# Kernel optimization log

Measured on AMD Instinct MI355X. Metric: run time of the kernel, lower is better.

Reference implementation:

```python
import jax, jax.numpy as jnp
import numpy as np

N_NODES = 50000
N_EDGES = 640000
IN_CH = 64
EDGE_DIM = 16
HID = 128
OUT = 128
L = 5
N_GRAPHS = 128
BN_EPS = 1e-5


def setup_inputs() -> dict:
    key = jax.random.key(0)
    ks = jax.random.split(key, 16)

    def w(k, shape, fan_in):
        return jax.random.normal(k, shape, jnp.float32) / np.sqrt(fan_in)

    inp = {}
    inp["x"] = jax.random.normal(ks[0], (N_NODES, IN_CH), jnp.float32)
    inp["edge_index"] = jax.random.randint(ks[1], (2, N_EDGES), 0, N_NODES)
    inp["edge_attr"] = jax.random.normal(ks[2], (N_EDGES, EDGE_DIM), jnp.float32)
    inp["batch"] = jnp.sort(jax.random.randint(ks[3], (N_NODES,), 0, N_GRAPHS))
    # node / edge encoders
    inp["node_w"] = w(ks[4], (IN_CH, HID), IN_CH)
    inp["node_b"] = jnp.zeros((HID,), jnp.float32)
    inp["edge_w"] = w(ks[5], (EDGE_DIM, HID), EDGE_DIM)
    inp["edge_b"] = jnp.zeros((HID,), jnp.float32)
    # per-layer GINEConv params (stacked over L layers)
    inp["eps"] = jnp.zeros((L,), jnp.float32)  # train_eps init 0
    inp["lin_w"] = w(ks[6], (L, HID, HID), HID)       # GINEConv internal edge lin
    inp["lin_b"] = jnp.zeros((L, HID), jnp.float32)
    inp["mlp1_w"] = w(ks[7], (L, HID, 2 * HID), HID)
    inp["mlp1_b"] = jnp.zeros((L, 2 * HID), jnp.float32)
    inp["mlp2_w"] = w(ks[8], (L, 2 * HID, HID), 2 * HID)
    inp["mlp2_b"] = jnp.zeros((L, HID), jnp.float32)
    inp["bn_g"] = jnp.ones((L, HID), jnp.float32)
    inp["bn_b"] = jnp.zeros((L, HID), jnp.float32)
    # output MLP: HID -> HID//2 -> OUT
    inp["out_w1"] = w(ks[9], (HID, HID // 2), HID)
    inp["out_b1"] = jnp.zeros((HID // 2,), jnp.float32)
    inp["out_w2"] = w(ks[10], (HID // 2, OUT), HID // 2)
    inp["out_b2"] = jnp.zeros((OUT,), jnp.float32)
    return inp


def reference(x, edge_index, edge_attr, batch, node_w, node_b, edge_w, edge_b,
              eps, lin_w, lin_b, mlp1_w, mlp1_b, mlp2_w, mlp2_b, bn_g, bn_b,
              out_w1, out_b1, out_w2, out_b2):
    n_nodes = x.shape[0]
    src, dst = edge_index[0], edge_index[1]
    # node / edge encoders (dropout is identity in eval)
    h = jax.nn.relu(x @ node_w + node_b)            # [N, H]
    e = edge_attr @ edge_w + edge_b                  # [E, H]
    n_layers = lin_w.shape[0]
    for l in range(n_layers):
        # GINEConv: message = relu(x_src + lin(edge_emb)); aggregate = scatter-sum to dst
        m = jax.nn.relu(h[src] + e @ lin_w[l] + lin_b[l])      # [E, H]
        agg = jax.ops.segment_sum(m, dst, num_segments=n_nodes)  # [N, H]
        z = (1.0 + eps[l]) * h + agg
        # GINE MLP: H -> 2H -> H
        z = jax.nn.relu(z @ mlp1_w[l] + mlp1_b[l]) @ mlp2_w[l] + mlp2_b[l]
        # BatchNorm over nodes (training-mode batch statistics)
        mu = z.mean(axis=0)
        var = z.var(axis=0)
        z = (z - mu) * jax.lax.rsqrt(var + BN_EPS) * bn_g[l] + bn_b[l]
        # residual then relu
        h = jax.nn.relu(z + h)
    # global mean pool per graph
    counts = jax.ops.segment_sum(jnp.ones((n_nodes,), h.dtype), batch, num_segments=N_GRAPHS)
    pooled = jax.ops.segment_sum(h, batch, num_segments=N_GRAPHS) / jnp.maximum(counts, 1.0)[:, None]
    # output MLP (dropout identity in eval)
    logits = jax.nn.relu(pooled @ out_w1 + out_b1) @ out_w2 + out_b2
    return (logits, pooled)
```

## Files before the change

### kernel.cpp

```cpp
#include <hip/hip_runtime.h>

#define N_NODES  50000
#define NPAD     50048
#define N_EDGES  640000
#define IN_CH    64
#define EDGE_DIM 16
#define HID      128
#define HID2     256
#define NLAYER   5
#define NGRAPH   128
#define MT64     (NPAD / 64)

typedef unsigned short ushort_t;
typedef __attribute__((ext_vector_type(8))) short short8;
typedef __attribute__((ext_vector_type(4))) short s16x4;
typedef __attribute__((ext_vector_type(4))) float f32x4;
typedef __attribute__((ext_vector_type(2))) float f32x2;

__device__ __forceinline__ float b2f(ushort_t u) {
    union { unsigned v; float f; } x; x.v = ((unsigned)u) << 16; return x.f;
}
__device__ __forceinline__ ushort_t f2b(float f) {
    union { float f; unsigned u; } x; x.f = f;
    unsigned u = x.u;
    unsigned r = (u + 0x7FFFu + ((u >> 16) & 1u)) >> 16;
    return (ushort_t)r;
}

__global__ void k_transpose_cvt(const float* __restrict__ src, ushort_t* __restrict__ dst,
                                int B, int K, int Nn) {
    long total = (long)B * K * Nn;
    for (long i = (long)blockIdx.x * blockDim.x + threadIdx.x; i < total;
         i += (long)gridDim.x * blockDim.x) {
        int b = (int)(i / ((long)K * Nn));
        int rem = (int)(i - (long)b * K * Nn);
        int k = rem / Nn;
        int n = rem - k * Nn;
        dst[(long)b * K * Nn + (long)n * K + k] = f2b(src[i]);
    }
}

__global__ __launch_bounds__(128) void k_combine(const float* __restrict__ ew,
                                                 const float* __restrict__ eb,
                                                 const float* __restrict__ lw,
                                                 const float* __restrict__ lb,
                                                 ushort_t* __restrict__ WcbT,
                                                 float* __restrict__ cc) {
    int l = blockIdx.x, j = threadIdx.x;
    float accW[EDGE_DIM];
#pragma unroll
    for (int k = 0; k < EDGE_DIM; ++k) accW[k] = 0.f;
    float accc = 0.f;
    for (int i = 0; i < HID; ++i) {
        float lwv = lw[((long)l * HID + i) * HID + j];
        accc = fmaf(eb[i], lwv, accc);
#pragma unroll
        for (int k = 0; k < EDGE_DIM; ++k)
            accW[k] = fmaf(ew[k * HID + i], lwv, accW[k]);
    }
    ushort_t* wp = WcbT + ((long)l * HID + j) * 32;
#pragma unroll
    for (int k = 0; k < EDGE_DIM; ++k) wp[k] = f2b(accW[k]);
#pragma unroll
    for (int k = EDGE_DIM; k < 32; ++k) wp[k] = 0;
    cc[l * HID + j] = accc + lb[l * HID + j];
}

__global__ __launch_bounds__(256) void k_hist(const int* __restrict__ ei, int* __restrict__ deg) {
    int e = blockIdx.x * 256 + threadIdx.x;
    if (e < N_EDGES) atomicAdd(&deg[ei[N_EDGES + e]], 1);
}

__global__ __launch_bounds__(1024) void k_scan1(const int* __restrict__ deg,
                                                int* __restrict__ offs, int* __restrict__ bsum) {
    __shared__ int s[1024];
    int i = blockIdx.x * 1024 + threadIdx.x;
    int v = (i < N_NODES) ? deg[i] : 0;
    s[threadIdx.x] = v;
    __syncthreads();
    for (int off = 1; off < 1024; off <<= 1) {
        int t = (threadIdx.x >= off) ? s[threadIdx.x - off] : 0;
        __syncthreads();
        s[threadIdx.x] += t;
        __syncthreads();
    }
    if (i < N_NODES) offs[i] = s[threadIdx.x] - v;
    if (threadIdx.x == 1023) bsum[blockIdx.x] = s[1023];
}

__global__ void k_scan2(int* __restrict__ bsum, int nb) {
    if (threadIdx.x == 0 && blockIdx.x == 0) {
        int acc = 0;
        for (int i = 0; i < nb; ++i) { int v = bsum[i]; bsum[i] = acc; acc += v; }
    }
}

__global__ __launch_bounds__(1024) void k_scan3(int* __restrict__ offs, const int* __restrict__ bsum) {
    int i = blockIdx.x * 1024 + threadIdx.x;
    if (i < N_NODES) offs[i] += bsum[blockIdx.x];
}

__global__ __launch_bounds__(256) void k_scatter(const int* __restrict__ ei,
                                                 const float* __restrict__ ea,
                                                 const int* __restrict__ offs,
                                                 int* __restrict__ cursor,
                                                 int* __restrict__ src_s,
                                                 ushort_t* __restrict__ ea_sb) {
    int e = blockIdx.x * 256 + threadIdx.x;
    if (e >= N_EDGES) return;
    int d = ei[N_EDGES + e];
    int pos = offs[d] + atomicAdd(&cursor[d], 1);
    src_s[pos] = ei[e];
    const f32x4* srcp = (const f32x4*)(ea + (long)e * EDGE_DIM);
    f32x4 v0 = srcp[0], v1 = srcp[1], v2 = srcp[2], v3 = srcp[3];
    short8 o0, o1;
#pragma unroll
    for (int j = 0; j < 4; ++j) {
        o0[j] = (short)f2b(v0[j]); o0[4 + j] = (short)f2b(v1[j]);
        o1[j] = (short)f2b(v2[j]); o1[4 + j] = (short)f2b(v3[j]);
    }
    short8* dst = (short8*)(ea_sb + (long)pos * EDGE_DIM);
    dst[0] = o0;
    dst[1] = o1;
}

__global__ __launch_bounds__(256) void k_node_enc(const float* __restrict__ x,
                                                  const ushort_t* __restrict__ w0T,
                                                  const float* __restrict__ nb,
                                                  float* __restrict__ h,
                                                  ushort_t* __restrict__ hb) {
    __shared__ __align__(16) short lB[HID * IN_CH];
    for (int c = threadIdx.x; c < HID * IN_CH / 8; c += 256) {
        int row = c >> 3, k0 = (c & 7) * 8;
        short8 v = *(const short8*)(w0T + row * IN_CH + k0);
        int g = (k0 >> 3) ^ (row & 7);
        *(short8*)&lB[row * IN_CH + g * 8] = v;
    }
    __syncthreads();
    int wv = threadIdx.x >> 6, l6 = threadIdx.x & 63;
    int lr = l6 & 15, lg = l6 >> 4;
    int grow = blockIdx.x * 64 + wv * 16 + lr;
    f32x4 acc[8];
#pragma unroll
    for (int nt = 0; nt < 8; ++nt) acc[nt] = (f32x4){0.f, 0.f, 0.f, 0.f};
#pragma unroll
    for (int kt = 0; kt < 2; ++kt) {
        int kk = kt * 32 + lg * 8;
        short8 a = {0, 0, 0, 0, 0, 0, 0, 0};
        if (grow < N_NODES) {
            const float* xr = x + (long)grow * IN_CH + kk;
            f32x4 v0 = *(const f32x4*)xr;
            f32x4 v1 = *(const f32x4*)(xr + 4);
#pragma unroll
            for (int j = 0; j < 4; ++j) { a[j] = (short)f2b(v0[j]); a[4 + j] = (short)f2b(v1[j]); }
        }
#pragma unroll
        for (int nt = 0; nt < 8; ++nt) {
            int brow = nt * 16 + lr;
            short8 b = *(const short8*)&lB[brow * IN_CH + (((kk >> 3) ^ (brow & 7)) << 3)];
            acc[nt] = __builtin_amdgcn_mfma_f32_16x16x32_bf16(a, b, acc[nt], 0, 0, 0);
        }
    }
    int orow0 = blockIdx.x * 64 + wv * 16 + lg * 4;
#pragma unroll
    for (int nt = 0; nt < 8; ++nt) {
        int col = nt * 16 + lr;
        float bias = nb[col];
#pragma unroll
        for (int r = 0; r < 4; ++r) {
            int row = orow0 + r;
            if (row < N_NODES) {
                float v = fmaxf(acc[nt][r] + bias, 0.f);
                h[(long)row * HID + col] = v;
                hb[(long)row * HID + col] = f2b(v);
            }
        }
    }
}

__global__ __launch_bounds__(256) void k_edgegemm(const ushort_t* __restrict__ ea_sb,
                                                  const ushort_t* __restrict__ WcbT,
                                                  const float* __restrict__ cc,
                                                  ushort_t* __restrict__ g, int l,
                                                  int ce0, int ce1) {
    int wv = threadIdx.x >> 6, l6 = threadIdx.x & 63;
    int lr = l6 & 15, lg = l6 >> 4;
    short8 af[8];
    f32x4 cv[8];
    const ushort_t* wp = WcbT + (long)l * HID * 32;
#pragma unroll
    for (int nt = 0; nt < 8; ++nt) {
        af[nt] = *(const short8*)(wp + (nt * 16 + lr) * 32 + lg * 8);
        cv[nt] = *(const f32x4*)(cc + l * HID + nt * 16 + lg * 4);
    }
    for (int it = 0; it < 4; ++it) {
        int e0 = ce0 + blockIdx.x * 256 + wv * 64 + it * 16;
        int e = e0 + lr;
        short8 b = {0, 0, 0, 0, 0, 0, 0, 0};
        if (e < ce1 && lg < 2) b = *(const short8*)(ea_sb + (long)e * EDGE_DIM + lg * 8);
        f32x4 acc[8];
#pragma unroll
        for (int nt = 0; nt < 8; ++nt) acc[nt] = (f32x4){0.f, 0.f, 0.f, 0.f};
#pragma unroll
        for (int nt = 0; nt < 8; ++nt)
            acc[nt] = __builtin_amdgcn_mfma_f32_16x16x32_bf16(af[nt], b, acc[nt], 0, 0, 0);
        if (e < ce1) {
            ushort_t* gp = g + (long)(e - ce0) * HID + lg * 4;
#pragma unroll
            for (int nt = 0; nt < 8; ++nt) {
                s16x4 o;
#pragma unroll
                for (int r = 0; r < 4; ++r) o[r] = (short)f2b(acc[nt][r] + cv[nt][r]);
                *(s16x4*)(gp + nt * 16) = o;
            }
        }
    }
}

__global__ __launch_bounds__(256) void k_edge2(const ushort_t* __restrict__ g,
                                               const int* __restrict__ src_s,
                                               const int* __restrict__ offs,
                                               const int* __restrict__ deg,
                                               const float* __restrict__ h,
                                               const ushort_t* __restrict__ hb,
                                               const float* __restrict__ epsv,
                                               float* __restrict__ zacc,
                                               ushort_t* __restrict__ z,
                                               int l, int ce0, int ce1, int mode) {
    int lane = threadIdx.x & 63;
    int node = blockIdx.x * 4 + (threadIdx.x >> 6);
    if (node >= N_NODES) return;
    bool first = mode & 1, last = (mode & 2) != 0;
    int ch0 = lane * 2;
    int s0 = offs[node];
    int dg = deg[node];
    int e_lo = max(s0, ce0);
    int e_hi = min(s0 + dg, ce1);
    if (e_lo >= e_hi && !first && !last) return;
    float a0 = 0.f, a1 = 0.f;
    int i = e_lo;
    for (; i + 4 <= e_hi; i += 4) {
        long eg = (long)(i - ce0);
        int sa = src_s[i], sb_ = src_s[i + 1], sc_ = src_s[i + 2], sd_ = src_s[i + 3];
        unsigned ga = *(const unsigned*)(g + eg * HID + ch0);
        unsigned gb = *(const unsigned*)(g + (eg + 1) * HID + ch0);
        unsigned gc = *(const unsigned*)(g + (eg + 2) * HID + ch0);
        unsigned gd = *(const unsigned*)(g + (eg + 3) * HID + ch0);
        unsigned ha = *(const unsigned*)(hb + (long)sa * HID + ch0);
        unsigned hbv = *(const unsigned*)(hb + (long)sb_ * HID + ch0);
        unsigned hc = *(const unsigned*)(hb + (long)sc_ * HID + ch0);
        unsigned hd = *(const unsigned*)(hb + (long)sd_ * HID + ch0);
        a0 += fmaxf(b2f((ushort_t)(ha & 0xffff)) + b2f((ushort_t)(ga & 0xffff)), 0.f);
        a1 += fmaxf(b2f((ushort_t)(ha >> 16)) + b2f((ushort_t)(ga >> 16)), 0.f);
        a0 += fmaxf(b2f((ushort_t)(hbv & 0xffff)) + b2f((ushort_t)(gb & 0xffff)), 0.f);
        a1 += fmaxf(b2f((ushort_t)(hbv >> 16)) + b2f((ushort_t)(gb >> 16)), 0.f);
        a0 += fmaxf(b2f((ushort_t)(hc & 0xffff)) + b2f((ushort_t)(gc & 0xffff)), 0.f);
        a1 += fmaxf(b2f((ushort_t)(hc >> 16)) + b2f((ushort_t)(gc >> 16)), 0.f);
        a0 += fmaxf(b2f((ushort_t)(hd & 0xffff)) + b2f((ushort_t)(gd & 0xffff)), 0.f);
        a1 += fmaxf(b2f((ushort_t)(hd >> 16)) + b2f((ushort_t)(gd >> 16)), 0.f);
    }
    for (; i < e_hi; ++i) {
        long eg = (long)(i - ce0);
        int s = src_s[i];
        unsigned gv = *(const unsigned*)(g + eg * HID + ch0);
        unsigned hv = *(const unsigned*)(hb + (long)s * HID + ch0);
        a0 += fmaxf(b2f((ushort_t)(hv & 0xffff)) + b2f((ushort_t)(gv & 0xffff)), 0.f);
        a1 += fmaxf(b2f((ushort_t)(hv >> 16)) + b2f((ushort_t)(gv >> 16)), 0.f);
    }
    if (!first) {
        f32x2 p = *(const f32x2*)(zacc + (long)node * HID + ch0);
        a0 += p[0]; a1 += p[1];
    }
    if (last) {
        float ep1 = 1.f + epsv[l];
        f32x2 hn = *(const f32x2*)(h + (long)node * HID + ch0);
        unsigned zz = (unsigned)f2b(fmaf(ep1, hn[0], a0)) |
                      ((unsigned)f2b(fmaf(ep1, hn[1], a1)) << 16);
        *(unsigned*)(z + (long)node * HID + ch0) = zz;
    } else {
        *(f32x2*)(zacc + (long)node * HID + ch0) = (f32x2){a0, a1};
    }
}

__global__ __launch_bounds__(256) void k_mlp1(const ushort_t* __restrict__ z,
                                              const ushort_t* __restrict__ w1T,
                                              const float* __restrict__ b1,
                                              ushort_t* __restrict__ ibuf, int l) {
    __shared__ __align__(16) short lBw[128 * HID];
    int half = blockIdx.x & 1;
    int tile = blockIdx.x >> 1;
    const ushort_t* wl = w1T + (long)l * HID2 * HID + (long)half * 128 * HID;
    for (int c = threadIdx.x; c < 128 * HID / 8; c += 256) {
        int row = c >> 4, k0 = (c & 15) * 8;
        short8 v = *(const short8*)(wl + row * HID + k0);
        int gsw = (k0 >> 3) ^ (row & 7);
        *(short8*)&lBw[row * HID + gsw * 8] = v;
    }
    int wv = threadIdx.x >> 6, l6 = threadIdx.x & 63;
    int lr = l6 & 15, lg = l6 >> 4;
    int node = tile * 64 + wv * 16 + lr;
    short8 b[4];
    const ushort_t* zr = z + (long)node * HID;
#pragma unroll
    for (int kt = 0; kt < 4; ++kt) b[kt] = *(const short8*)(zr + kt * 32 + lg * 8);
    __syncthreads();
#pragma unroll
    for (int nt = 0; nt < 8; ++nt) {
        f32x4 acc = (f32x4){0.f, 0.f, 0.f, 0.f};
        int brow = nt * 16 + lr;
#pragma unroll
        for (int kt = 0; kt < 4; ++kt) {
            short8 af = *(const short8*)&lBw[brow * HID + (((kt * 4 + lg) ^ (brow & 7)) << 3)];
            acc = __builtin_amdgcn_mfma_f32_16x16x32_bf16(af, b[kt], acc, 0, 0, 0);
        }
        f32x4 bv = *(const f32x4*)(b1 + l * HID2 + half * 128 + nt * 16 + lg * 4);
        s16x4 o;
#pragma unroll
        for (int r = 0; r < 4; ++r) o[r] = (short)f2b(fmaxf(acc[r] + bv[r], 0.f));
        *(s16x4*)(ibuf + (long)node * HID2 + half * 128 + nt * 16 + lg * 4) = o;
    }
}

__global__ __launch_bounds__(256) void k_mlp2(const ushort_t* __restrict__ ibuf,
                                              const ushort_t* __restrict__ w2T,
                                              const float* __restrict__ b2,
                                              ushort_t* __restrict__ z2,
                                              float* __restrict__ bnstats, int l) {
    __shared__ __align__(16) short lBw[64 * HID2];
    __shared__ float lStat[2][64];
    int half = blockIdx.x & 1;
    int tile = blockIdx.x >> 1;
    const ushort_t* wl = w2T + (long)l * HID * HID2 + (long)half * 64 * HID2;
    for (int c = threadIdx.x; c < 64 * HID2 / 8; c += 256) {
        int row = c >> 5, k0 = (c & 31) * 8;
        short8 v = *(const short8*)(wl + row * HID2 + k0);
        int gsw = (k0 >> 3) ^ (row & 7);
        *(short8*)&lBw[row * HID2 + gsw * 8] = v;
    }
    if (threadIdx.x < 128) lStat[threadIdx.x >> 6][threadIdx.x & 63] = 0.f;
    int wv = threadIdx.x >> 6, l6 = threadIdx.x & 63;
    int lr = l6 & 15, lg = l6 >> 4;
    int node = tile * 64 + wv * 16 + lr;
    bool valid = node < N_NODES;
    short8 b[8];
    const ushort_t* ir = ibuf + (long)node * HID2;
#pragma unroll
    for (int kt = 0; kt < 8; ++kt) b[kt] = *(const short8*)(ir + kt * 32 + lg * 8);
    __syncthreads();
#pragma unroll
    for (int nt = 0; nt < 4; ++nt) {
        f32x4 acc = (f32x4){0.f, 0.f, 0.f, 0.f};
        int brow = nt * 16 + lr;
#pragma unroll
        for (int kt = 0; kt < 8; ++kt) {
            short8 af = *(const short8*)&lBw[brow * HID2 + (((kt * 4 + lg) ^ (brow & 7)) << 3)];
            acc = __builtin_amdgcn_mfma_f32_16x16x32_bf16(af, b[kt], acc, 0, 0, 0);
        }
        f32x4 bv = *(const f32x4*)(b2 + l * HID + half * 64 + nt * 16 + lg * 4);
        s16x4 o;
#pragma unroll
        for (int r = 0; r < 4; ++r) {
            float v = acc[r] + bv[r];
            o[r] = (short)f2b(v);
            float s = valid ? v : 0.f, q = valid ? v * v : 0.f;
            s += __shfl_xor(s, 1); s += __shfl_xor(s, 2);
            s += __shfl_xor(s, 4); s += __shfl_xor(s, 8);
            q += __shfl_xor(q, 1); q += __shfl_xor(q, 2);
            q += __shfl_xor(q, 4); q += __shfl_xor(q, 8);
            if (lr == 0) {
                int f = nt * 16 + lg * 4 + r;
                atomicAdd(&lStat[0][f], s);
                atomicAdd(&lStat[1][f], q);
            }
        }
        *(s16x4*)(z2 + (long)node * HID + half * 64 + nt * 16 + lg * 4) = o;
    }
    __syncthreads();
    if (threadIdx.x < 128) {
        int which = threadIdx.x >> 6, f = threadIdx.x & 63;
        atomicAdd(&bnstats[(which * NLAYER + l) * HID + half * 64 + f], lStat[which][f]);
    }
}

__global__ __launch_bounds__(1024) void k_resid(const ushort_t* __restrict__ z2,
                                                const float* __restrict__ bnstats,
                                                const float* __restrict__ bng,
                                                const float* __restrict__ bnb,
                                                float* __restrict__ h,
                                                ushort_t* __restrict__ hb, int l) {
    long i = (long)blockIdx.x * 1024 + threadIdx.x;
    int c = (int)(i & (HID - 1));
    float inv = 1.f / (float)N_NODES;
    float mu = bnstats[l * HID + c] * inv;
    float var = bnstats[(NLAYER + l) * HID + c] * inv - mu * mu;
    float A = rsqrtf(var + 1e-5f) * bng[l * HID + c];
    float B = bnb[l * HID + c] - mu * A;
    float v = fmaf(b2f(z2[i]), A, B) + h[i];
    v = fmaxf(v, 0.f);
    h[i] = v;
    hb[i] = f2b(v);
}

__global__ void k_gstart(const int* __restrict__ batch, int* __restrict__ gstart) {
    int g = threadIdx.x;
    if (g > NGRAPH) return;
    int lo = 0, hi = N_NODES;
    while (lo < hi) { int mid = (lo + hi) >> 1; if (batch[mid] < g) lo = mid + 1; else hi = mid; }
    gstart[g] = lo;
}

__global__ __launch_bounds__(512) void k_pool(const float* __restrict__ h,
                                              const int* __restrict__ gstart,
                                              float* __restrict__ pooled,
                                              float* __restrict__ outp) {
    __shared__ float red[4][HID];
    int g = blockIdx.x;
    int ch = threadIdx.x & 127, seg = threadIdx.x >> 7;
    int st = gstart[g], en = gstart[g + 1];
    float s = 0.f;
    for (int i = st + seg; i < en; i += 4) s += h[(long)i * HID + ch];
    red[seg][ch] = s;
    __syncthreads();
    if (seg == 0) {
        float p = (red[0][ch] + red[1][ch] + red[2][ch] + red[3][ch]) /
                  fmaxf((float)(en - st), 1.f);
        pooled[g * HID + ch] = p;
        outp[g * HID + ch] = p;
    }
}

__global__ __launch_bounds__(128) void k_outmlp(const float* __restrict__ pooled,
                                                const float* __restrict__ w1,
                                                const float* __restrict__ b1,
                                                const float* __restrict__ w2,
                                                const float* __restrict__ b2,
                                                float* __restrict__ outl) {
    __shared__ float pr[HID];
    __shared__ float hid[64];
    int g = blockIdx.x, t = threadIdx.x;
    pr[t] = pooled[g * HID + t];
    __syncthreads();
    if (t < 64) {
        float a = b1[t];
        for (int k = 0; k < HID; ++k) a = fmaf(pr[k], w1[k * 64 + t], a);
        hid[t] = fmaxf(a, 0.f);
    }
    __syncthreads();
    float a = b2[t];
#pragma unroll
    for (int j = 0; j < 64; ++j) a = fmaf(hid[j], w2[j * HID + t], a);
    outl[g * HID + t] = a;
}

extern "C" void kernel_launch(void* const* d_in, const int* in_sizes, int n_in,
                              void* d_out, int out_size, void* d_ws, size_t ws_size,
                              hipStream_t stream) {
    (void)in_sizes; (void)n_in; (void)out_size;
    const float* x      = (const float*)d_in[0];
    const int*   ei     = (const int*)d_in[1];
    const float* ea     = (const float*)d_in[2];
    const int*   batch  = (const int*)d_in[3];
    const float* node_w = (const float*)d_in[4];
    const float* node_b = (const float*)d_in[5];
    const float* edge_w = (const float*)d_in[6];
    const float* edge_b = (const float*)d_in[7];
    const float* epsv   = (const float*)d_in[8];
    const float* lin_w  = (const float*)d_in[9];
    const float* lin_b  = (const float*)d_in[10];
    const float* m1w    = (const float*)d_in[11];
    const float* m1b    = (const float*)d_in[12];
    const float* m2w    = (const float*)d_in[13];
    const float* m2b    = (const float*)d_in[14];
    const float* bng    = (const float*)d_in[15];
    const float* bnb    = (const float*)d_in[16];
    const float* ow1    = (const float*)d_in[17];
    const float* ob1    = (const float*)d_in[18];
    const float* ow2    = (const float*)d_in[19];
    const float* ob2    = (const float*)d_in[20];

    const size_t MiB = 1024ull * 1024ull;
    int NC;
    if      (ws_size >= 275 * MiB) NC = 1;
    else if (ws_size >= 193 * MiB) NC = 2;
    else if (ws_size >= 152 * MiB) NC = 4;
    else                           NC = 8;
    int EC = (N_EDGES + NC - 1) / NC;

    char* ws = (char*)d_ws;
    size_t off = 0;
    auto alloc = [&](size_t bytes) -> char* {
        char* p = ws + off;
        off = (off + bytes + 255) & ~(size_t)255;
        return p;
    };
    float*    h       = (float*)alloc((size_t)NPAD * HID * 4);
    ushort_t* hb      = (ushort_t*)alloc((size_t)NPAD * HID * 2);
    ushort_t* z       = (ushort_t*)alloc((size_t)NPAD * HID * 2);
    ushort_t* ibuf    = (ushort_t*)alloc((size_t)NPAD * HID2 * 2);
    ushort_t* ea_sb   = (ushort_t*)alloc((size_t)N_EDGES * EDGE_DIM * 2 + 64);
    ushort_t* g       = (ushort_t*)alloc((size_t)EC * HID * 2);
    int*      src_s   = (int*)alloc((size_t)N_EDGES * 4);
    int*      deg     = (int*)alloc((size_t)N_NODES * 4);
    int*      offs    = (int*)alloc((size_t)N_NODES * 4);
    int*      cursor  = (int*)alloc((size_t)N_NODES * 4);
    int*      bsum    = (int*)alloc(64 * 4);
    ushort_t* WcbT    = (ushort_t*)alloc((size_t)NLAYER * HID * 32 * 2);
    float*    cc      = (float*)alloc((size_t)NLAYER * HID * 4);
    ushort_t* w0T     = (ushort_t*)alloc((size_t)HID * IN_CH * 2);
    ushort_t* w1T     = (ushort_t*)alloc((size_t)NLAYER * HID2 * HID * 2);
    ushort_t* w2T     = (ushort_t*)alloc((size_t)NLAYER * HID * HID2 * 2);
    float*    bnstats = (float*)alloc((size_t)2 * NLAYER * HID * 4);
    int*      gstart  = (int*)alloc((NGRAPH + 1) * 4);
    float*    pooled  = (float*)alloc((size_t)NGRAPH * HID * 4);
    float*    zacc    = (float*)ibuf;
    ushort_t* z2      = z;

    (void)hipMemsetAsync(deg, 0, (size_t)N_NODES * 4, stream);
    (void)hipMemsetAsync(cursor, 0, (size_t)N_NODES * 4, stream);
    (void)hipMemsetAsync(bnstats, 0, (size_t)2 * NLAYER * HID * 4, stream);

    k_transpose_cvt<<<64, 256, 0, stream>>>(node_w, w0T, 1, IN_CH, HID);
    k_transpose_cvt<<<640, 256, 0, stream>>>(m1w, w1T, NLAYER, HID, HID2);
    k_transpose_cvt<<<640, 256, 0, stream>>>(m2w, w2T, NLAYER, HID2, HID);
    k_combine<<<NLAYER, HID, 0, stream>>>(edge_w, edge_b, lin_w, lin_b, WcbT, cc);

    k_hist<<<N_EDGES / 256, 256, 0, stream>>>(ei, deg);
    k_scan1<<<49, 1024, 0, stream>>>(deg, offs, bsum);
    k_scan2<<<1, 1, 0, stream>>>(bsum, 49);
    k_scan3<<<49, 1024, 0, stream>>>(offs, bsum);
    k_scatter<<<N_EDGES / 256, 256, 0, stream>>>(ei, ea, offs, cursor, src_s, ea_sb);

    k_node_enc<<<NPAD / 64, 256, 0, stream>>>(x, w0T, node_b, h, hb);

    for (int l = 0; l < NLAYER; ++l) {
        for (int c = 0; c < NC; ++c) {
            int ce0 = c * EC;
            int ce1 = (ce0 + EC < N_EDGES) ? (ce0 + EC) : N_EDGES;
            int nblk = (ce1 - ce0 + 255) / 256;
            int mode = (c == 0 ? 1 : 0) | (c == NC - 1 ? 2 : 0);
            k_edgegemm<<<nblk, 256, 0, stream>>>(ea_sb, WcbT, cc, g, l, ce0, ce1);
            k_edge2<<<(N_NODES + 3) / 4, 256, 0, stream>>>(g, src_s, offs, deg, h, hb,
                                                           epsv, zacc, z, l, ce0, ce1, mode);
        }
        k_mlp1<<<MT64 * 2, 256, 0, stream>>>(z, w1T, m1b, ibuf, l);
        k_mlp2<<<MT64 * 2, 256, 0, stream>>>(ibuf, w2T, m2b, z2, bnstats, l);
        k_resid<<<(N_NODES * HID) / 1024, 1024, 0, stream>>>(z2, bnstats, bng, bnb, h, hb, l);
    }

    k_gstart<<<1, 256, 0, stream>>>(batch, gstart);
    k_pool<<<NGRAPH, 512, 0, stream>>>(h, gstart, pooled, (float*)d_out + NGRAPH * HID);
    k_outmlp<<<NGRAPH, HID, 0, stream>>>(pooled, ow1, ob1, ow2, ob2, (float*)d_out);
}
```

Measured before the change: 1.079 ms.

## Fuse edge-embedding GEMM with message aggregation through LDS, split edge sort

Edge projection and aggregation now run in one kernel per layer, replacing the separate edge GEMM and gather kernels. Each block computes the projected edge features for 256 destination-sorted edges into LDS, then aggregates them per destination node. This removes the large global intermediate buffer and its chunking loop. Nodes whose edges cross block boundaries go through float atomics into a zeroed accumulator, and a finalize kernel writes and clears those. The edge sort is also split into a permutation pass and a separate gather pass, so converted edge attributes are written contiguously. In exchange, each block uses 64 KB of LDS, which limits occupancy, and boundary nodes pay for atomics.

```diff
diff --git a/kernel.cpp b/kernel.cpp
--- a/kernel.cpp
+++ b/kernel.cpp
@@ -10,6 +10,7 @@
 #define NLAYER   5
 #define NGRAPH   128
 #define MT64     (NPAD / 64)
+#define EPB      256
 
 typedef unsigned short ushort_t;
 typedef __attribute__((ext_vector_type(8))) short short8;
@@ -100,17 +101,26 @@
     if (i < N_NODES) offs[i] += bsum[blockIdx.x];
 }
 
-__global__ __launch_bounds__(256) void k_scatter(const int* __restrict__ ei,
-                                                 const float* __restrict__ ea,
-                                                 const int* __restrict__ offs,
-                                                 int* __restrict__ cursor,
-                                                 int* __restrict__ src_s,
-                                                 ushort_t* __restrict__ ea_sb) {
+__global__ __launch_bounds__(256) void k_scatter1(const int* __restrict__ ei,
+                                                  const int* __restrict__ offs,
+                                                  int* __restrict__ cursor,
+                                                  int* __restrict__ perm) {
     int e = blockIdx.x * 256 + threadIdx.x;
     if (e >= N_EDGES) return;
     int d = ei[N_EDGES + e];
     int pos = offs[d] + atomicAdd(&cursor[d], 1);
-    src_s[pos] = ei[e];
+    perm[pos] = e;
+}
+
+__global__ __launch_bounds__(256) void k_gather(const int* __restrict__ perm,
+                                                const int* __restrict__ ei,
+                                                const float* __restrict__ ea,
+                                                int* __restrict__ src_s,
+                                                ushort_t* __restrict__ ea_sb) {
+    int p = blockIdx.x * 256 + threadIdx.x;
+    if (p >= N_EDGES) return;
+    int e = perm[p];
+    src_s[p] = ei[e];
     const f32x4* srcp = (const f32x4*)(ea + (long)e * EDGE_DIM);
     f32x4 v0 = srcp[0], v1 = srcp[1], v2 = srcp[2], v3 = srcp[3];
     short8 o0, o1;
@@ -119,7 +129,7 @@
         o0[j] = (short)f2b(v0[j]); o0[4 + j] = (short)f2b(v1[j]);
         o1[j] = (short)f2b(v2[j]); o1[4 + j] = (short)f2b(v3[j]);
     }
-    short8* dst = (short8*)(ea_sb + (long)pos * EDGE_DIM);
+    short8* dst = (short8*)(ea_sb + (long)p * EDGE_DIM);
     dst[0] = o0;
     dst[1] = o1;
 }
@@ -178,108 +188,137 @@
     }
 }
 
-__global__ __launch_bounds__(256) void k_edgegemm(const ushort_t* __restrict__ ea_sb,
-                                                  const ushort_t* __restrict__ WcbT,
-                                                  const float* __restrict__ cc,
-                                                  ushort_t* __restrict__ g, int l,
-                                                  int ce0, int ce1) {
+__global__ __launch_bounds__(256) void k_edgefused(const ushort_t* __restrict__ ea_sb,
+                                                   const ushort_t* __restrict__ WcbT,
+                                                   const float* __restrict__ cc,
+                                                   const int* __restrict__ src_s,
+                                                   const int* __restrict__ offs,
+                                                   const int* __restrict__ deg,
+                                                   const float* __restrict__ h,
+                                                   const ushort_t* __restrict__ hb,
+                                                   const float* __restrict__ epsv,
+                                                   float* __restrict__ zacc,
+                                                   ushort_t* __restrict__ z, int l) {
+    __shared__ __align__(16) ushort_t lG[EPB * HID];
+    __shared__ int sNode[2];
+    int p0 = blockIdx.x * EPB;
+    int p1 = p0 + EPB < N_EDGES ? p0 + EPB : N_EDGES;
     int wv = threadIdx.x >> 6, l6 = threadIdx.x & 63;
     int lr = l6 & 15, lg = l6 >> 4;
-    short8 af[8];
-    f32x4 cv[8];
-    const ushort_t* wp = WcbT + (long)l * HID * 32;
-#pragma unroll
-    for (int nt = 0; nt < 8; ++nt) {
-        af[nt] = *(const short8*)(wp + (nt * 16 + lr) * 32 + lg * 8);
-        cv[nt] = *(const f32x4*)(cc + l * HID + nt * 16 + lg * 4);
-    }
-    for (int it = 0; it < 4; ++it) {
-        int e0 = ce0 + blockIdx.x * 256 + wv * 64 + it * 16;
-        int e = e0 + lr;
-        short8 b = {0, 0, 0, 0, 0, 0, 0, 0};
-        if (e < ce1 && lg < 2) b = *(const short8*)(ea_sb + (long)e * EDGE_DIM + lg * 8);
-        f32x4 acc[8];
-#pragma unroll
-        for (int nt = 0; nt < 8; ++nt) acc[nt] = (f32x4){0.f, 0.f, 0.f, 0.f};
-#pragma unroll
-        for (int nt = 0; nt < 8; ++nt)
-            acc[nt] = __builtin_amdgcn_mfma_f32_16x16x32_bf16(af[nt], b, acc[nt], 0, 0, 0);
-        if (e < ce1) {
-            ushort_t* gp = g + (long)(e - ce0) * HID + lg * 4;
-#pragma unroll
-            for (int nt = 0; nt < 8; ++nt) {
-                s16x4 o;
-#pragma unroll
-                for (int r = 0; r < 4; ++r) o[r] = (short)f2b(acc[nt][r] + cv[nt][r]);
-                *(s16x4*)(gp + nt * 16) = o;
+
+    if (threadIdx.x == 0) {
+        int lo = 0, hi = N_NODES - 1;
+        while (lo < hi) { int mid = (lo + hi + 1) >> 1; if (offs[mid] <= p0) lo = mid; else hi = mid - 1; }
+        sNode[0] = lo;
+        int pm = p1 - 1;
+        lo = 0; hi = N_NODES - 1;
+        while (lo < hi) { int mid = (lo + hi + 1) >> 1; if (offs[mid] <= pm) lo = mid; else hi = mid - 1; }
+        sNode[1] = lo;
+    }
+
+    {
+        short8 af[8];
+        f32x4 cv[8];
+        const ushort_t* wp = WcbT + (long)l * HID * 32;
+#pragma unroll
+        for (int nt = 0; nt < 8; ++nt) {
+            af[nt] = *(const short8*)(wp + (nt * 16 + lr) * 32 + lg * 8);
+            cv[nt] = *(const f32x4*)(cc + l * HID + nt * 16 + lg * 4);
+        }
+#pragma unroll
+        for (int it = 0; it < 4; ++it) {
+            int e = p0 + wv * 64 + it * 16 + lr;
+            short8 b = {0, 0, 0, 0, 0, 0, 0, 0};
+            if (e < p1 && lg < 2) b = *(const short8*)(ea_sb + (long)e * EDGE_DIM + lg * 8);
+            f32x4 acc[8];
+#pragma unroll
+            for (int nt = 0; nt < 8; ++nt) acc[nt] = (f32x4){0.f, 0.f, 0.f, 0.f};
+#pragma unroll
+            for (int nt = 0; nt < 8; ++nt)
+                acc[nt] = __builtin_amdgcn_mfma_f32_16x16x32_bf16(af[nt], b, acc[nt], 0, 0, 0);
+            if (e < p1) {
+                int el = e - p0;
+#pragma unroll
+                for (int nt = 0; nt < 8; ++nt) {
+                    int chb = nt * 16 + lg * 4;
+                    int chs = chb ^ ((el & 7) << 2);
+                    s16x4 o;
+#pragma unroll
+                    for (int r = 0; r < 4; ++r) o[r] = (short)f2b(acc[nt][r] + cv[nt][r]);
+                    *(s16x4*)&lG[el * HID + chs] = o;
+                }
             }
         }
     }
-}
-
-__global__ __launch_bounds__(256) void k_edge2(const ushort_t* __restrict__ g,
-                                               const int* __restrict__ src_s,
-                                               const int* __restrict__ offs,
-                                               const int* __restrict__ deg,
-                                               const float* __restrict__ h,
-                                               const ushort_t* __restrict__ hb,
-                                               const float* __restrict__ epsv,
-                                               float* __restrict__ zacc,
-                                               ushort_t* __restrict__ z,
-                                               int l, int ce0, int ce1, int mode) {
+    __syncthreads();
+
+    int n_lo = sNode[0], n_hi = sNode[1];
+    int ch0 = l6 * 2;
+    int base4 = ch0 & ~3, coff = ch0 & 3;
+    float ep1 = 1.f + epsv[l];
+    for (int n = n_lo + wv; n <= n_hi; n += 4) {
+        int o_n = offs[n], d_n = deg[n];
+        int e_lo = o_n > p0 ? o_n : p0;
+        int e_hi = (o_n + d_n) < p1 ? (o_n + d_n) : p1;
+        float a0 = 0.f, a1 = 0.f;
+        int i = e_lo;
+        for (; i + 4 <= e_hi; i += 4) {
+            int sa = src_s[i], sb_ = src_s[i + 1], sc_ = src_s[i + 2], sd_ = src_s[i + 3];
+            unsigned ha = *(const unsigned*)(hb + (long)sa * HID + ch0);
+            unsigned hbv = *(const unsigned*)(hb + (long)sb_ * HID + ch0);
+            unsigned hc = *(const unsigned*)(hb + (long)sc_ * HID + ch0);
+            unsigned hd = *(const unsigned*)(hb + (long)sd_ * HID + ch0);
+#pragma unroll
+            for (int j = 0; j < 4; ++j) {
+                int el = i + j - p0;
+                unsigned gv = *(const unsigned*)&lG[el * HID + (base4 ^ ((el & 7) << 2)) + coff];
+                unsigned hv = (j == 0) ? ha : (j == 1) ? hbv : (j == 2) ? hc : hd;
+                a0 += fmaxf(b2f((ushort_t)(hv & 0xffff)) + b2f((ushort_t)(gv & 0xffff)), 0.f);
+                a1 += fmaxf(b2f((ushort_t)(hv >> 16)) + b2f((ushort_t)(gv >> 16)), 0.f);
+            }
+        }
+        for (; i < e_hi; ++i) {
+            int s = src_s[i];
+            unsigned hv = *(const unsigned*)(hb + (long)s * HID + ch0);
+            int el = i - p0;
+            unsigned gv = *(const unsigned*)&lG[el * HID + (base4 ^ ((el & 7) << 2)) + coff];
+            a0 += fmaxf(b2f((ushort_t)(hv & 0xffff)) + b2f((ushort_t)(gv & 0xffff)), 0.f);
+            a1 += fmaxf(b2f((ushort_t)(hv >> 16)) + b2f((ushort_t)(gv >> 16)), 0.f);
+        }
+        bool interior = (o_n >= p0) && (o_n + d_n <= p1);
+        if (interior) {
+            f32x2 hn = *(const f32x2*)(h + (long)n * HID + ch0);
+            unsigned zz = (unsigned)f2b(fmaf(ep1, hn[0], a0)) |
+                          ((unsigned)f2b(fmaf(ep1, hn[1], a1)) << 16);
+            *(unsigned*)(z + (long)n * HID + ch0) = zz;
+        } else if (e_lo < e_hi) {
+            atomicAdd(&zacc[(long)n * HID + ch0], a0);
+            atomicAdd(&zacc[(long)n * HID + ch0 + 1], a1);
+        }
+    }
+}
+
+__global__ __launch_bounds__(256) void k_edgefin(const int* __restrict__ offs,
+                                                 const int* __restrict__ deg,
+                                                 const float* __restrict__ h,
+                                                 const float* __restrict__ epsv,
+                                                 float* __restrict__ zacc,
+                                                 ushort_t* __restrict__ z, int l) {
     int lane = threadIdx.x & 63;
     int node = blockIdx.x * 4 + (threadIdx.x >> 6);
     if (node >= N_NODES) return;
-    bool first = mode & 1, last = (mode & 2) != 0;
+    int o = offs[node], d = deg[node];
+    bool boundary = (d == 0) || ((o / EPB) != ((o + d - 1) / EPB));
+    if (!boundary) return;
     int ch0 = lane * 2;
-    int s0 = offs[node];
-    int dg = deg[node];
-    int e_lo = max(s0, ce0);
-    int e_hi = min(s0 + dg, ce1);
-    if (e_lo >= e_hi && !first && !last) return;
-    float a0 = 0.f, a1 = 0.f;
-    int i = e_lo;
-    for (; i + 4 <= e_hi; i += 4) {
-        long eg = (long)(i - ce0);
-        int sa = src_s[i], sb_ = src_s[i + 1], sc_ = src_s[i + 2], sd_ = src_s[i + 3];
-        unsigned ga = *(const unsigned*)(g + eg * HID + ch0);
-        unsigned gb = *(const unsigned*)(g + (eg + 1) * HID + ch0);
-        unsigned gc = *(const unsigned*)(g + (eg + 2) * HID + ch0);
-        unsigned gd = *(const unsigned*)(g + (eg + 3) * HID + ch0);
-        unsigned ha = *(const unsigned*)(hb + (long)sa * HID + ch0);
-        unsigned hbv = *(const unsigned*)(hb + (long)sb_ * HID + ch0);
-        unsigned hc = *(const unsigned*)(hb + (long)sc_ * HID + ch0);
-        unsigned hd = *(const unsigned*)(hb + (long)sd_ * HID + ch0);
-        a0 += fmaxf(b2f((ushort_t)(ha & 0xffff)) + b2f((ushort_t)(ga & 0xffff)), 0.f);
-        a1 += fmaxf(b2f((ushort_t)(ha >> 16)) + b2f((ushort_t)(ga >> 16)), 0.f);
-        a0 += fmaxf(b2f((ushort_t)(hbv & 0xffff)) + b2f((ushort_t)(gb & 0xffff)), 0.f);
-        a1 += fmaxf(b2f((ushort_t)(hbv >> 16)) + b2f((ushort_t)(gb >> 16)), 0.f);
-        a0 += fmaxf(b2f((ushort_t)(hc & 0xffff)) + b2f((ushort_t)(gc & 0xffff)), 0.f);
-        a1 += fmaxf(b2f((ushort_t)(hc >> 16)) + b2f((ushort_t)(gc >> 16)), 0.f);
-        a0 += fmaxf(b2f((ushort_t)(hd & 0xffff)) + b2f((ushort_t)(gd & 0xffff)), 0.f);
-        a1 += fmaxf(b2f((ushort_t)(hd >> 16)) + b2f((ushort_t)(gd >> 16)), 0.f);
-    }
-    for (; i < e_hi; ++i) {
-        long eg = (long)(i - ce0);
-        int s = src_s[i];
-        unsigned gv = *(const unsigned*)(g + eg * HID + ch0);
-        unsigned hv = *(const unsigned*)(hb + (long)s * HID + ch0);
-        a0 += fmaxf(b2f((ushort_t)(hv & 0xffff)) + b2f((ushort_t)(gv & 0xffff)), 0.f);
-        a1 += fmaxf(b2f((ushort_t)(hv >> 16)) + b2f((ushort_t)(gv >> 16)), 0.f);
-    }
-    if (!first) {
-        f32x2 p = *(const f32x2*)(zacc + (long)node * HID + ch0);
-        a0 += p[0]; a1 += p[1];
-    }
-    if (last) {
-        float ep1 = 1.f + epsv[l];
-        f32x2 hn = *(const f32x2*)(h + (long)node * HID + ch0);
-        unsigned zz = (unsigned)f2b(fmaf(ep1, hn[0], a0)) |
-                      ((unsigned)f2b(fmaf(ep1, hn[1], a1)) << 16);
-        *(unsigned*)(z + (long)node * HID + ch0) = zz;
-    } else {
-        *(f32x2*)(zacc + (long)node * HID + ch0) = (f32x2){a0, a1};
-    }
+    long base = (long)node * HID + ch0;
+    f32x2 za = *(const f32x2*)(zacc + base);
+    float ep1 = 1.f + epsv[l];
+    f32x2 hn = *(const f32x2*)(h + base);
+    unsigned zz = (unsigned)f2b(fmaf(ep1, hn[0], za[0])) |
+                  ((unsigned)f2b(fmaf(ep1, hn[1], za[1])) << 16);
+    *(unsigned*)(z + base) = zz;
+    *(f32x2*)(zacc + base) = (f32x2){0.f, 0.f};
 }
 
 __global__ __launch_bounds__(256) void k_mlp1(const ushort_t* __restrict__ z,
@@ -455,7 +494,7 @@
 extern "C" void kernel_launch(void* const* d_in, const int* in_sizes, int n_in,
                               void* d_out, int out_size, void* d_ws, size_t ws_size,
                               hipStream_t stream) {
-    (void)in_sizes; (void)n_in; (void)out_size;
+    (void)in_sizes; (void)n_in; (void)out_size; (void)ws_size;
     const float* x      = (const float*)d_in[0];
     const int*   ei     = (const int*)d_in[1];
     const float* ea     = (const float*)d_in[2];
@@ -478,14 +517,6 @@
     const float* ow2    = (const float*)d_in[19];
     const float* ob2    = (const float*)d_in[20];
 
-    const size_t MiB = 1024ull * 1024ull;
-    int NC;
-    if      (ws_size >= 275 * MiB) NC = 1;
-    else if (ws_size >= 193 * MiB) NC = 2;
-    else if (ws_size >= 152 * MiB) NC = 4;
-    else                           NC = 8;
-    int EC = (N_EDGES + NC - 1) / NC;
-
     char* ws = (char*)d_ws;
     size_t off = 0;
     auto alloc = [&](size_t bytes) -> char* {
@@ -497,8 +528,8 @@
     ushort_t* hb      = (ushort_t*)alloc((size_t)NPAD * HID * 2);
     ushort_t* z       = (ushort_t*)alloc((size_t)NPAD * HID * 2);
     ushort_t* ibuf    = (ushort_t*)alloc((size_t)NPAD * HID2 * 2);
+    float*    zacc    = (float*)alloc((size_t)NPAD * HID * 4);
     ushort_t* ea_sb   = (ushort_t*)alloc((size_t)N_EDGES * EDGE_DIM * 2 + 64);
-    ushort_t* g       = (ushort_t*)alloc((size_t)EC * HID * 2);
     int*      src_s   = (int*)alloc((size_t)N_EDGES * 4);
     int*      deg     = (int*)alloc((size_t)N_NODES * 4);
     int*      offs    = (int*)alloc((size_t)N_NODES * 4);
@@ -512,12 +543,13 @@
     float*    bnstats = (float*)alloc((size_t)2 * NLAYER * HID * 4);
     int*      gstart  = (int*)alloc((NGRAPH + 1) * 4);
     float*    pooled  = (float*)alloc((size_t)NGRAPH * HID * 4);
-    float*    zacc    = (float*)ibuf;
+    int*      perm    = (int*)ibuf;
     ushort_t* z2      = z;
 
     (void)hipMemsetAsync(deg, 0, (size_t)N_NODES * 4, stream);
     (void)hipMemsetAsync(cursor, 0, (size_t)N_NODES * 4, stream);
     (void)hipMemsetAsync(bnstats, 0, (size_t)2 * NLAYER * HID * 4, stream);
+    (void)hipMemsetAsync(zacc, 0, (size_t)NPAD * HID * 4, stream);
 
     k_transpose_cvt<<<64, 256, 0, stream>>>(node_w, w0T, 1, IN_CH, HID);
     k_transpose_cvt<<<640, 256, 0, stream>>>(m1w, w1T, NLAYER, HID, HID2);
@@ -528,20 +560,16 @@
     k_scan1<<<49, 1024, 0, stream>>>(deg, offs, bsum);
     k_scan2<<<1, 1, 0, stream>>>(bsum, 49);
     k_scan3<<<49, 1024, 0, stream>>>(offs, bsum);
-    k_scatter<<<N_EDGES / 256, 256, 0, stream>>>(ei, ea, offs, cursor, src_s, ea_sb);
+    k_scatter1<<<N_EDGES / 256, 256, 0, stream>>>(ei, offs, cursor, perm);
+    k_gather<<<N_EDGES / 256, 256, 0, stream>>>(perm, ei, ea, src_s, ea_sb);
 
     k_node_enc<<<NPAD / 64, 256, 0, stream>>>(x, w0T, node_b, h, hb);
 
+    int nfused = (N_EDGES + EPB - 1) / EPB;
     for (int l = 0; l < NLAYER; ++l) {
-        for (int c = 0; c < NC; ++c) {
-            int ce0 = c * EC;
-            int ce1 = (ce0 + EC < N_EDGES) ? (ce0 + EC) : N_EDGES;
-            int nblk = (ce1 - ce0 + 255) / 256;
-            int mode = (c == 0 ? 1 : 0) | (c == NC - 1 ? 2 : 0);
-            k_edgegemm<<<nblk, 256, 0, stream>>>(ea_sb, WcbT, cc, g, l, ce0, ce1);
-            k_edge2<<<(N_NODES + 3) / 4, 256, 0, stream>>>(g, src_s, offs, deg, h, hb,
-                                                           epsv, zacc, z, l, ce0, ce1, mode);
-        }
+        k_edgefused<<<nfused, 256, 0, stream>>>(ea_sb, WcbT, cc, src_s, offs, deg,
+                                                h, hb, epsv, zacc, z, l);
+        k_edgefin<<<(N_NODES + 3) / 4, 256, 0, stream>>>(offs, deg, h, epsv, zacc, z, l);
         k_mlp1<<<MT64 * 2, 256, 0, stream>>>(z, w1T, m1b, ibuf, l);
         k_mlp2<<<MT64 * 2, 256, 0, stream>>>(ibuf, w2T, m2b, z2, bnstats, l);
         k_resid<<<(N_NODES * HID) / 1024, 1024, 0, stream>>>(z2, bnstats, bng, bnb, h, hb, l);
```

Measured after the change: 1.197 ms. 1.11x slower.
